# Performance work log

Measured on AMD Instinct MI355X. Metric: run time of the kernel, lower is better.

Reference implementation:

```python
import jax, jax.numpy as jnp
import numpy as np

STRIDE = 1
PAD = 1
DIL = 1


def setup_inputs() -> dict:
    key = jax.random.key(0)
    k1, k2, k3, k4 = jax.random.split(key, 4)
    N, Cin, H, W = 4, 256, 64, 64
    Cout, kh, kw = 256, 3, 3
    inputs = jax.random.normal(k1, (N, Cin, H, W), jnp.float32)
    filter = jax.random.normal(k2, (Cout, Cin, kh, kw), jnp.float32) * 0.05
    # offsets in pixels (y,x interleaved per tap), typical magnitude O(1)
    offset = jax.random.normal(k3, (N, 2 * kh * kw, H, W), jnp.float32)
    # modulation mask in [0,1) (post-sigmoid in real nets)
    mask = jax.random.uniform(k4, (N, kh * kw, H, W), jnp.float32)
    return {"inputs": inputs, "filter": filter, "offset": offset, "mask": mask}


def _dcn_forward(inputs, filt, offset, mask):
    N, C, H, W = inputs.shape
    Cout, _, kh, kw = filt.shape
    K = kh * kw
    Ho = (H + 2 * PAD - DIL * (kh - 1) - 1) // STRIDE + 1
    Wo = (W + 2 * PAD - DIL * (kw - 1) - 1) // STRIDE + 1

    # base sampling grid per kernel tap: [K, Ho, Wo]
    ki, kj = jnp.meshgrid(jnp.arange(kh), jnp.arange(kw), indexing='ij')
    ki = ki.reshape(K, 1, 1)
    kj = kj.reshape(K, 1, 1)
    base_y = (jnp.arange(Ho)[None, :, None] * STRIDE - PAD + ki * DIL).astype(jnp.float32)
    base_x = (jnp.arange(Wo)[None, None, :] * STRIDE - PAD + kj * DIL).astype(jnp.float32)

    # offset channels: per tap k, channel 2k = dy, channel 2k+1 = dx
    off = offset.reshape(N, K, 2, Ho, Wo)
    y = base_y[None] + off[:, :, 0]  # [N, K, Ho, Wo]
    x = base_x[None] + off[:, :, 1]

    y0 = jnp.floor(y)
    x0 = jnp.floor(x)
    ly = y - y0  # fractional parts, [N, K, Ho, Wo]
    lx = x - x0
    y0i = y0.astype(jnp.int32)
    x0i = x0.astype(jnp.int32)

    def gather(img, yy, xx):
        # img [C,H,W]; yy,xx [K,Ho,Wo] int; zero outside bounds
        valid = (yy >= 0) & (yy < H) & (xx >= 0) & (xx < W)
        yc = jnp.clip(yy, 0, H - 1)
        xc = jnp.clip(xx, 0, W - 1)
        return img[:, yc, xc] * valid.astype(img.dtype)  # [C,K,Ho,Wo]

    def sample_one(img, y0i, x0i, ly, lx):
        v00 = gather(img, y0i, x0i)
        v01 = gather(img, y0i, x0i + 1)
        v10 = gather(img, y0i + 1, x0i)
        v11 = gather(img, y0i + 1, x0i + 1)
        return (v00 * (1 - ly) * (1 - lx) + v01 * (1 - ly) * lx
                + v10 * ly * (1 - lx) + v11 * ly * lx)

    # bilinear-sampled, modulated im2col columns: [N, C, K, Ho, Wo]
    col = jax.vmap(sample_one)(inputs, y0i, x0i, ly, lx)
    col = col * mask.reshape(N, 1, K, Ho, Wo)

    # grouped conv with num_groups=1: plain GEMM over (C, K)
    out = jnp.einsum('ock,nckhw->nohw', filt.reshape(Cout, C, K), col)
    return out


def reference(inputs, filter, offset, mask):
    return _dcn_forward(inputs, filter, offset, mask)
```

## Files before the change

### kernel.cpp

```cpp
#include <hip/hip_runtime.h>
#include <stdint.h>

typedef __attribute__((ext_vector_type(2))) float f32x2;
typedef __attribute__((ext_vector_type(4))) float f32x4;
typedef __attribute__((ext_vector_type(8))) short bf16x8;

static constexpr int N_ = 4, C_ = 256, HW_ = 4096;
static constexpr int CO_ = 256, KTAP = 9, KK = 2304;
static constexpr int NSTEP = 72;
static constexpr int A_STEP_BYTES = 16 * 64 * 16;

static constexpr size_t NHWC_BYTES = (size_t)N_ * HW_ * C_ * 2;
static constexpr size_t ABF_OFF    = NHWC_BYTES;
static constexpr size_t ABF_BYTES  = (size_t)NSTEP * A_STEP_BYTES;

__device__ inline unsigned f2bf(float f) {
  unsigned u = __builtin_bit_cast(unsigned, f);
  unsigned r = u + 0x7FFFu + ((u >> 16) & 1u);
  return r >> 16;
}
__device__ inline float asf(unsigned u) { return __builtin_bit_cast(float, u); }

__global__ __launch_bounds__(256) void k_nchw_to_nhwc(const float* __restrict__ in,
                                                      unsigned short* __restrict__ nhwc) {
  __shared__ float tile[64][65];
  int b = blockIdx.x;
  int n = b >> 8, cg = (b >> 6) & 3, hwg = b & 63;
  int c0 = cg * 64, hw0 = hwg * 64;
  int t = threadIdx.x;
  int col = t & 63, r0 = t >> 6;
#pragma unroll
  for (int i = 0; i < 16; ++i) {
    int row = r0 + i * 4;
    tile[row][col] = in[(size_t)(n * C_ + c0 + row) * HW_ + hw0 + col];
  }
  __syncthreads();
  int pr = t >> 2, cc0 = (t & 3) * 16;
  unsigned us[8];
#pragma unroll
  for (int i = 0; i < 8; ++i) {
    unsigned lo = f2bf(tile[cc0 + 2 * i][pr]);
    unsigned hi = f2bf(tile[cc0 + 2 * i + 1][pr]);
    us[i] = lo | (hi << 16);
  }
  unsigned* dst = (unsigned*)(nhwc + (size_t)(n * HW_ + hw0 + pr) * C_ + c0 + cc0);
  ((uint4*)dst)[0] = make_uint4(us[0], us[1], us[2], us[3]);
  ((uint4*)dst)[1] = make_uint4(us[4], us[5], us[6], us[7]);
}

__global__ __launch_bounds__(256) void k_prep_filter(const float* __restrict__ filt,
                                                     unsigned short* __restrict__ abf2) {
  int gid = blockIdx.x * 256 + threadIdx.x;
  int o = gid >> 8, c = gid & 255;
  const float* f = filt + (size_t)(o * C_ + c) * KTAP;
  int rb = o >> 4;
  int lane = ((c >> 3) & 3) * 16 + (o & 15);
  int j = c & 7;
#pragma unroll
  for (int tap = 0; tap < KTAP; ++tap) {
    int s = tap * 8 + (c >> 5);
    abf2[((size_t)(s * 16 + rb) * 64 + lane) * 8 + j] = (unsigned short)f2bf(f[tap]);
  }
}

struct GB { uint4 g[4]; f32x4 w; };

__device__ __forceinline__ f32x2 unpk(unsigned u) {
  return (f32x2){asf(u << 16), asf(u & 0xffff0000u)};
}

__device__ __forceinline__ void buildB8(const GB& b, char* dst) {
  f32x2 r0 = b.w.x * unpk(b.g[0].x) + b.w.y * unpk(b.g[1].x) +
             b.w.z * unpk(b.g[2].x) + b.w.w * unpk(b.g[3].x);
  f32x2 r1 = b.w.x * unpk(b.g[0].y) + b.w.y * unpk(b.g[1].y) +
             b.w.z * unpk(b.g[2].y) + b.w.w * unpk(b.g[3].y);
  f32x2 r2 = b.w.x * unpk(b.g[0].z) + b.w.y * unpk(b.g[1].z) +
             b.w.z * unpk(b.g[2].z) + b.w.w * unpk(b.g[3].z);
  f32x2 r3 = b.w.x * unpk(b.g[0].w) + b.w.y * unpk(b.g[1].w) +
             b.w.z * unpk(b.g[2].w) + b.w.w * unpk(b.g[3].w);
  unsigned o0, o1, o2, o3;
  asm("v_cvt_pk_bf16_f32 %0, %1, %2" : "=v"(o0) : "v"(r0.x), "v"(r0.y));
  asm("v_cvt_pk_bf16_f32 %0, %1, %2" : "=v"(o1) : "v"(r1.x), "v"(r1.y));
  asm("v_cvt_pk_bf16_f32 %0, %1, %2" : "=v"(o2) : "v"(r2.x), "v"(r2.y));
  asm("v_cvt_pk_bf16_f32 %0, %1, %2" : "=v"(o3) : "v"(r3.x), "v"(r3.y));
  *(uint4*)dst = make_uint4(o0, o1, o2, o3);
}

#define MFMA_BF16 __builtin_amdgcn_mfma_f32_16x16x32_bf16

#define PIPE(S, RDP, WRP, GCON, GISS, AC0, AC1, AN0, AN1)                      \
  do {                                                                         \
    if (cons) {                                                                \
      int s1_ = (S) + 1 < NSTEP ? (S) + 1 : NSTEP - 1;                         \
      AN0 = *(const bf16x8*)(aoff0 + (size_t)s1_ * A_STEP_BYTES);              \
      AN1 = *(const bf16x8*)(aoff1 + (size_t)s1_ * A_STEP_BYTES);              \
      const char* bb_ = (const char*)&Bl[0][0] + (RDP) * 4096;                 \
      bf16x8 b0_ = *(const bf16x8*)(bb_ + bo0);                                \
      bf16x8 b1_ = *(const bf16x8*)(bb_ + bo1);                                \
      __builtin_amdgcn_s_setprio(1);                                           \
      acc[0][0] = MFMA_BF16(AC0, b0_, acc[0][0], 0, 0, 0);                     \
      acc[1][0] = MFMA_BF16(AC1, b0_, acc[1][0], 0, 0, 0);                     \
      acc[0][1] = MFMA_BF16(AC0, b1_, acc[0][1], 0, 0, 0);                     \
      acc[1][1] = MFMA_BF16(AC1, b1_, acc[1][1], 0, 0, 0);                     \
      __builtin_amdgcn_s_setprio(0);                                           \
      bf16x8 b2_ = *(const bf16x8*)(bb_ + bo2);                                \
      bf16x8 b3_ = *(const bf16x8*)(bb_ + bo3);                                \
      __builtin_amdgcn_s_setprio(1);                                           \
      acc[0][2] = MFMA_BF16(AC0, b2_, acc[0][2], 0, 0, 0);                     \
      acc[1][2] = MFMA_BF16(AC1, b2_, acc[1][2], 0, 0, 0);                     \
      acc[0][3] = MFMA_BF16(AC0, b3_, acc[0][3], 0, 0, 0);                     \
      acc[1][3] = MFMA_BF16(AC1, b3_, acc[1][3], 0, 0, 0);                     \
      __builtin_amdgcn_s_setprio(0);                                           \
    } else {                                                                   \
      int s2_ = (S) + 2 < NSTEP ? (S) + 2 : NSTEP - 1;                         \
      if ((s2_ & 7) == 0) {                                                    \
        int tp_ = s2_ >> 3;                                                    \
        uint4 ra_ = *(const uint4*)&recA[(tp_ * 64 + p_b) * 4];                \
        wS = *(const f32x4*)&recW[(tp_ * 64 + p_b) * 4];                       \
        vS.x = ra_.x + kq16; vS.y = ra_.y + kq16;                              \
        vS.z = ra_.z + kq16; vS.w = ra_.w + kq16;                              \
      }                                                                        \
      unsigned co_ = (unsigned)((s2_ & 7) * 64);                               \
      GISS.g[0] = *(const uint4*)(nb_u + vS.x + co_);                          \
      GISS.g[1] = *(const uint4*)(nb_u + vS.y + co_);                          \
      GISS.g[2] = *(const uint4*)(nb_u + vS.z + co_);                          \
      GISS.g[3] = *(const uint4*)(nb_u + vS.w + co_);                          \
      GISS.w = wS;                                                             \
      buildB8(GCON, bwp + (WRP) * 4096);                                       \
      asm volatile("s_waitcnt lgkmcnt(0)" ::: "memory");                       \
    }                                                                          \
    asm volatile("" ::: "memory");                                             \
    __builtin_amdgcn_s_barrier();                                              \
    asm volatile("" ::: "memory");                                             \
  } while (0)

__global__ __launch_bounds__(768, 3) void k_dcn_gemm(const unsigned short* __restrict__ nhwc,
                                                     const unsigned short* __restrict__ abf2,
                                                     const float* __restrict__ offs,
                                                     const float* __restrict__ msk,
                                                     float* __restrict__ out) {
  __shared__ __align__(16) unsigned short Bl[2][2048];
  __shared__ float recW[KTAP * 64 * 4];
  __shared__ unsigned recA[KTAP * 64 * 4];

  int bid = blockIdx.x;
  int b = ((bid & 7) << 5) | (bid >> 3);
  int n = b >> 6;
  int ho = b & 63;
  int hw0 = ho << 6;
  int t = threadIdx.x;

  for (int r = t; r < 576; r += 768) {
    int pl = r / 9;
    int tap = r - pl * 9;
    int hw = hw0 + pl;
    float dy = offs[(size_t)(n * 18 + 2 * tap) * HW_ + hw];
    float dx = offs[(size_t)(n * 18 + 2 * tap + 1) * HW_ + hw];
    float mk = msk[(size_t)(n * 9 + tap) * HW_ + hw];
    float y = (float)(ho - 1 + tap / 3) + dy;
    float x = (float)(pl - 1 + tap % 3) + dx;
    float fy = floorf(y), fx = floorf(x);
    float ly = y - fy, lx = x - fx;
    int y0 = (int)fy, x0 = (int)fx;
    int y1 = y0 + 1, x1 = x0 + 1;
    float vy0 = (y0 >= 0 && y0 < 64) ? 1.f : 0.f;
    float vy1 = (y1 >= 0 && y1 < 64) ? 1.f : 0.f;
    float vx0 = (x0 >= 0 && x0 < 64) ? 1.f : 0.f;
    float vx1 = (x1 >= 0 && x1 < 64) ? 1.f : 0.f;
    int y0c = min(max(y0, 0), 63), y1c = min(max(y1, 0), 63);
    int x0c = min(max(x0, 0), 63), x1c = min(max(x1, 0), 63);
    int base = (tap * 64 + pl) * 4;
    recW[base + 0] = (1.f - ly) * (1.f - lx) * mk * vy0 * vx0;
    recW[base + 1] = (1.f - ly) * lx * mk * vy0 * vx1;
    recW[base + 2] = ly * (1.f - lx) * mk * vy1 * vx0;
    recW[base + 3] = ly * lx * mk * vy1 * vx1;
    recA[base + 0] = (unsigned)((y0c * 64 + x0c) * 512);
    recA[base + 1] = (unsigned)((y0c * 64 + x1c) * 512);
    recA[base + 2] = (unsigned)((y1c * 64 + x0c) * 512);
    recA[base + 3] = (unsigned)((y1c * 64 + x1c) * 512);
  }
  __syncthreads();

  int lane = t & 63, wv = t >> 6;
  bool cons = wv < 8;

  const char* aoff0 = (const char*)abf2 + ((wv * 2 + 0) * 64 + lane) * 16;
  const char* aoff1 = aoff0 + 1024;
  int cqr = lane >> 4;
  int pxl = lane & 15;
  const int bo0 = cqr * 1024 + ((((0 * 16 + pxl) + cqr * 5) & 63) * 16);
  const int bo1 = cqr * 1024 + ((((1 * 16 + pxl) + cqr * 5) & 63) * 16);
  const int bo2 = cqr * 1024 + ((((2 * 16 + pxl) + cqr * 5) & 63) * 16);
  const int bo3 = cqr * 1024 + ((((3 * 16 + pxl) + cqr * 5) & 63) * 16);

  int p_b = (t >> 2) & 63;
  int kq = t & 3;
  unsigned kq16 = (unsigned)(kq * 16);
  const char* nb_u = (const char*)nhwc + (size_t)n * HW_ * C_ * 2;
  char* bwp = (char*)&Bl[0][0] + (kq * 1024 + ((p_b + kq * 5) & 63) * 16);

  f32x4 acc[2][4];
#pragma unroll
  for (int mi = 0; mi < 2; ++mi)
#pragma unroll
    for (int ni = 0; ni < 4; ++ni) acc[mi][ni] = (f32x4){0.f, 0.f, 0.f, 0.f};

  GB gA, gB;
  bf16x8 afc0, afc1, afn0, afn1;
  uint4 vS;
  f32x4 wS;

  if (cons) {
    afc0 = *(const bf16x8*)(aoff0);
    afc1 = *(const bf16x8*)(aoff1);
  } else {
    uint4 ra0 = *(const uint4*)&recA[p_b * 4];
    wS = *(const f32x4*)&recW[p_b * 4];
    vS.x = ra0.x + kq16; vS.y = ra0.y + kq16;
    vS.z = ra0.z + kq16; vS.w = ra0.w + kq16;
    gA.g[0] = *(const uint4*)(nb_u + vS.x);
    gA.g[1] = *(const uint4*)(nb_u + vS.y);
    gA.g[2] = *(const uint4*)(nb_u + vS.z);
    gA.g[3] = *(const uint4*)(nb_u + vS.w);
    gA.w = wS;
    gB.g[0] = *(const uint4*)(nb_u + vS.x + 64);
    gB.g[1] = *(const uint4*)(nb_u + vS.y + 64);
    gB.g[2] = *(const uint4*)(nb_u + vS.z + 64);
    gB.g[3] = *(const uint4*)(nb_u + vS.w + 64);
    gB.w = wS;
    buildB8(gA, bwp);
    asm volatile("s_waitcnt lgkmcnt(0)" ::: "memory");
  }
  asm volatile("" ::: "memory");
  __builtin_amdgcn_s_barrier();
  asm volatile("" ::: "memory");

  for (int s = 0; s < NSTEP; s += 2) {
    PIPE(s,     0, 1, gB, gA, afc0, afc1, afn0, afn1);
    PIPE(s + 1, 1, 0, gA, gB, afn0, afn1, afc0, afc1);
  }

  if (cons) {
    float* ob = out + (size_t)n * CO_ * HW_ + hw0;
#pragma unroll
    for (int mi = 0; mi < 2; ++mi)
#pragma unroll
      for (int ni = 0; ni < 4; ++ni)
#pragma unroll
        for (int jj = 0; jj < 4; ++jj) {
          int o = wv * 32 + mi * 16 + (lane >> 4) * 4 + jj;
          int hw = ni * 16 + (lane & 15);
          ob[(size_t)o * HW_ + hw] = acc[mi][ni][jj];
        }
  }
}

extern "C" void kernel_launch(void* const* d_in, const int* in_sizes, int n_in,
                              void* d_out, int out_size, void* d_ws, size_t ws_size,
                              hipStream_t stream) {
  const float* inp  = (const float*)d_in[0];
  const float* filt = (const float*)d_in[1];
  const float* offs = (const float*)d_in[2];
  const float* msk  = (const float*)d_in[3];
  float* out = (float*)d_out;
  if (ws_size < ABF_OFF + ABF_BYTES) return;
  unsigned short* nhwc = (unsigned short*)d_ws;
  unsigned short* abf2 = (unsigned short*)((char*)d_ws + ABF_OFF);

  k_nchw_to_nhwc<<<1024, 256, 0, stream>>>(inp, nhwc);
  k_prep_filter<<<256, 256, 0, stream>>>(filt, abf2);
  k_dcn_gemm<<<256, 768, 0, stream>>>(nhwc, abf2, offs, msk, out);
}
```

Measured before the change: 53.93 us.

## Split deformable sampling into separate kernel writing im2col to global memory

Adds a k_sample kernel that bilinearly samples and modulates the NHWC input into a global bf16 im2col buffer, then a k_gemm2 kernel that streams B tiles via global_load_lds into LDS and runs MFMA with 16 waves. The two prep kernels are merged into one launch, and the old fused kernel remains as a fallback when the workspace is too small. The aim is to decouple gather latency from the MFMA loop, at the cost of a large extra global write and read of the column buffer.

```diff
diff --git a/kernel.cpp b/kernel.cpp
--- a/kernel.cpp
+++ b/kernel.cpp
@@ -1,18 +1,24 @@
 #include <hip/hip_runtime.h>
 #include <stdint.h>
+
+#define AS1 __attribute__((address_space(1)))
+#define AS3 __attribute__((address_space(3)))
 
 typedef __attribute__((ext_vector_type(2))) float f32x2;
 typedef __attribute__((ext_vector_type(4))) float f32x4;
 typedef __attribute__((ext_vector_type(8))) short bf16x8;
 
 static constexpr int N_ = 4, C_ = 256, HW_ = 4096;
-static constexpr int CO_ = 256, KTAP = 9, KK = 2304;
+static constexpr int CO_ = 256, KTAP = 9;
 static constexpr int NSTEP = 72;
-static constexpr int A_STEP_BYTES = 16 * 64 * 16;
+static constexpr int A_PLANE = 16 * 64 * 16;
+static constexpr size_t TILE_STRIDE = 256 * 4096;
 
 static constexpr size_t NHWC_BYTES = (size_t)N_ * HW_ * C_ * 2;
 static constexpr size_t ABF_OFF    = NHWC_BYTES;
-static constexpr size_t ABF_BYTES  = (size_t)NSTEP * A_STEP_BYTES;
+static constexpr size_t ABF_BYTES  = (size_t)NSTEP * A_PLANE;
+static constexpr size_t BG_OFF     = ABF_OFF + ABF_BYTES;
+static constexpr size_t BG_BYTES   = (size_t)NSTEP * TILE_STRIDE;
 
 __device__ inline unsigned f2bf(float f) {
   unsigned u = __builtin_bit_cast(unsigned, f);
@@ -21,91 +27,225 @@
 }
 __device__ inline float asf(unsigned u) { return __builtin_bit_cast(float, u); }
 
-__global__ __launch_bounds__(256) void k_nchw_to_nhwc(const float* __restrict__ in,
-                                                      unsigned short* __restrict__ nhwc) {
-  __shared__ float tile[64][65];
+__global__ __launch_bounds__(256) void k_prep(const float* __restrict__ in,
+                                              const float* __restrict__ filt,
+                                              unsigned short* __restrict__ nhwc,
+                                              unsigned short* __restrict__ abf2) {
   int b = blockIdx.x;
-  int n = b >> 8, cg = (b >> 6) & 3, hwg = b & 63;
-  int c0 = cg * 64, hw0 = hwg * 64;
   int t = threadIdx.x;
-  int col = t & 63, r0 = t >> 6;
-#pragma unroll
-  for (int i = 0; i < 16; ++i) {
-    int row = r0 + i * 4;
-    tile[row][col] = in[(size_t)(n * C_ + c0 + row) * HW_ + hw0 + col];
-  }
-  __syncthreads();
-  int pr = t >> 2, cc0 = (t & 3) * 16;
-  unsigned us[8];
-#pragma unroll
-  for (int i = 0; i < 8; ++i) {
-    unsigned lo = f2bf(tile[cc0 + 2 * i][pr]);
-    unsigned hi = f2bf(tile[cc0 + 2 * i + 1][pr]);
-    us[i] = lo | (hi << 16);
-  }
-  unsigned* dst = (unsigned*)(nhwc + (size_t)(n * HW_ + hw0 + pr) * C_ + c0 + cc0);
-  ((uint4*)dst)[0] = make_uint4(us[0], us[1], us[2], us[3]);
-  ((uint4*)dst)[1] = make_uint4(us[4], us[5], us[6], us[7]);
-}
-
-__global__ __launch_bounds__(256) void k_prep_filter(const float* __restrict__ filt,
-                                                     unsigned short* __restrict__ abf2) {
-  int gid = blockIdx.x * 256 + threadIdx.x;
-  int o = gid >> 8, c = gid & 255;
-  const float* f = filt + (size_t)(o * C_ + c) * KTAP;
-  int rb = o >> 4;
-  int lane = ((c >> 3) & 3) * 16 + (o & 15);
-  int j = c & 7;
-#pragma unroll
-  for (int tap = 0; tap < KTAP; ++tap) {
-    int s = tap * 8 + (c >> 5);
-    abf2[((size_t)(s * 16 + rb) * 64 + lane) * 8 + j] = (unsigned short)f2bf(f[tap]);
-  }
-}
-
-struct GB { uint4 g[4]; f32x4 w; };
+  if (b < 1024) {
+    __shared__ float tile[64][65];
+    int n = b >> 8, cg = (b >> 6) & 3, hwg = b & 63;
+    int c0 = cg * 64, hw0 = hwg * 64;
+    int col = t & 63, r0 = t >> 6;
+#pragma unroll
+    for (int i = 0; i < 16; ++i) {
+      int row = r0 + i * 4;
+      tile[row][col] = in[(size_t)(n * C_ + c0 + row) * HW_ + hw0 + col];
+    }
+    __syncthreads();
+    int pr = t >> 2, cc0 = (t & 3) * 16;
+    unsigned us[8];
+#pragma unroll
+    for (int i = 0; i < 8; ++i) {
+      unsigned lo = f2bf(tile[cc0 + 2 * i][pr]);
+      unsigned hi = f2bf(tile[cc0 + 2 * i + 1][pr]);
+      us[i] = lo | (hi << 16);
+    }
+    unsigned* dst = (unsigned*)(nhwc + (size_t)(n * HW_ + hw0 + pr) * C_ + c0 + cc0);
+    ((uint4*)dst)[0] = make_uint4(us[0], us[1], us[2], us[3]);
+    ((uint4*)dst)[1] = make_uint4(us[4], us[5], us[6], us[7]);
+  } else {
+    int gid = (b - 1024) * 256 + t;
+    int o = gid >> 8, c = gid & 255;
+    const float* f = filt + (size_t)(o * C_ + c) * KTAP;
+    int rb = o >> 4;
+    int lane = ((c >> 3) & 3) * 16 + (o & 15);
+    int j = c & 7;
+#pragma unroll
+    for (int tap = 0; tap < KTAP; ++tap) {
+      int s = tap * 8 + (c >> 5);
+      abf2[((size_t)(s * 16 + rb) * 64 + lane) * 8 + j] = (unsigned short)f2bf(f[tap]);
+    }
+  }
+}
 
 __device__ __forceinline__ f32x2 unpk(unsigned u) {
   return (f32x2){asf(u << 16), asf(u & 0xffff0000u)};
 }
 
-__device__ __forceinline__ void buildB8(const GB& b, char* dst) {
-  f32x2 r0 = b.w.x * unpk(b.g[0].x) + b.w.y * unpk(b.g[1].x) +
-             b.w.z * unpk(b.g[2].x) + b.w.w * unpk(b.g[3].x);
-  f32x2 r1 = b.w.x * unpk(b.g[0].y) + b.w.y * unpk(b.g[1].y) +
-             b.w.z * unpk(b.g[2].y) + b.w.w * unpk(b.g[3].y);
-  f32x2 r2 = b.w.x * unpk(b.g[0].z) + b.w.y * unpk(b.g[1].z) +
-             b.w.z * unpk(b.g[2].z) + b.w.w * unpk(b.g[3].z);
-  f32x2 r3 = b.w.x * unpk(b.g[0].w) + b.w.y * unpk(b.g[1].w) +
-             b.w.z * unpk(b.g[2].w) + b.w.w * unpk(b.g[3].w);
+__device__ __forceinline__ uint4 comb8(const uint4& g0, const uint4& g1,
+                                       const uint4& g2, const uint4& g3, f32x4 w) {
+  f32x2 r0 = w.x * unpk(g0.x) + w.y * unpk(g1.x) + w.z * unpk(g2.x) + w.w * unpk(g3.x);
+  f32x2 r1 = w.x * unpk(g0.y) + w.y * unpk(g1.y) + w.z * unpk(g2.y) + w.w * unpk(g3.y);
+  f32x2 r2 = w.x * unpk(g0.z) + w.y * unpk(g1.z) + w.z * unpk(g2.z) + w.w * unpk(g3.z);
+  f32x2 r3 = w.x * unpk(g0.w) + w.y * unpk(g1.w) + w.z * unpk(g2.w) + w.w * unpk(g3.w);
   unsigned o0, o1, o2, o3;
   asm("v_cvt_pk_bf16_f32 %0, %1, %2" : "=v"(o0) : "v"(r0.x), "v"(r0.y));
   asm("v_cvt_pk_bf16_f32 %0, %1, %2" : "=v"(o1) : "v"(r1.x), "v"(r1.y));
   asm("v_cvt_pk_bf16_f32 %0, %1, %2" : "=v"(o2) : "v"(r2.x), "v"(r2.y));
   asm("v_cvt_pk_bf16_f32 %0, %1, %2" : "=v"(o3) : "v"(r3.x), "v"(r3.y));
-  *(uint4*)dst = make_uint4(o0, o1, o2, o3);
+  return make_uint4(o0, o1, o2, o3);
+}
+
+__global__ __launch_bounds__(512, 2) void k_sample(const unsigned short* __restrict__ nhwc,
+                                                   const float* __restrict__ offs,
+                                                   const float* __restrict__ msk,
+                                                   unsigned short* __restrict__ bglob) {
+  __shared__ f32x4 sW[64];
+  __shared__ uint4 sA[64];
+  int bid = blockIdx.x;
+  int b = (bid & 7) * 288 + (bid >> 3);
+  int row = b / 9, tap = b - row * 9;
+  int n = row >> 6, ho = row & 63;
+  int t = threadIdx.x;
+
+  if (t < 64) {
+    int pl = t, hw = ho * 64 + pl;
+    float dy = offs[(size_t)(n * 18 + 2 * tap) * HW_ + hw];
+    float dx = offs[(size_t)(n * 18 + 2 * tap + 1) * HW_ + hw];
+    float mk = msk[(size_t)(n * 9 + tap) * HW_ + hw];
+    float y = (float)(ho - 1 + tap / 3) + dy;
+    float x = (float)(pl - 1 + tap % 3) + dx;
+    float fy = floorf(y), fx = floorf(x);
+    float ly = y - fy, lx = x - fx;
+    int y0 = (int)fy, x0 = (int)fx;
+    int y1 = y0 + 1, x1 = x0 + 1;
+    float vy0 = (y0 >= 0 && y0 < 64) ? 1.f : 0.f;
+    float vy1 = (y1 >= 0 && y1 < 64) ? 1.f : 0.f;
+    float vx0 = (x0 >= 0 && x0 < 64) ? 1.f : 0.f;
+    float vx1 = (x1 >= 0 && x1 < 64) ? 1.f : 0.f;
+    int y0c = min(max(y0, 0), 63), y1c = min(max(y1, 0), 63);
+    int x0c = min(max(x0, 0), 63), x1c = min(max(x1, 0), 63);
+    sW[pl] = (f32x4){(1.f - ly) * (1.f - lx) * mk * vy0 * vx0,
+                     (1.f - ly) * lx * mk * vy0 * vx1,
+                     ly * (1.f - lx) * mk * vy1 * vx0,
+                     ly * lx * mk * vy1 * vx1};
+    sA[pl] = make_uint4((unsigned)((y0c * 64 + x0c) * 512),
+                        (unsigned)((y0c * 64 + x1c) * 512),
+                        (unsigned)((y1c * 64 + x0c) * 512),
+                        (unsigned)((y1c * 64 + x1c) * 512));
+  }
+  __syncthreads();
+
+  int px = t >> 3, cq = t & 7;
+  f32x4 w = sW[px];
+  uint4 ra = sA[px];
+  const char* nb = (const char*)nhwc + (size_t)n * HW_ * C_ * 2;
+  unsigned c16 = (unsigned)(cq * 16);
+
+  uint4 g0[4], g1[4], g2[4], g3[4];
+#pragma unroll
+  for (int j = 0; j < 4; ++j) {
+    unsigned o_ = (unsigned)(j * 128) + c16;
+    g0[j] = *(const uint4*)(nb + ra.x + o_);
+    g1[j] = *(const uint4*)(nb + ra.y + o_);
+    g2[j] = *(const uint4*)(nb + ra.z + o_);
+    g3[j] = *(const uint4*)(nb + ra.w + o_);
+  }
+
+  char* outb = (char*)bglob + (size_t)row * 4096 + px * 64 + (cq & 3) * 16;
+  int sbase = tap * 8 + (cq >> 2);
+#pragma unroll
+  for (int j = 0; j < 4; ++j) {
+    uint4 o4 = comb8(g0[j], g1[j], g2[j], g3[j], w);
+    *(uint4*)(outb + (size_t)(sbase + j * 2) * TILE_STRIDE) = o4;
+  }
 }
 
 #define MFMA_BF16 __builtin_amdgcn_mfma_f32_16x16x32_bf16
 
-#define PIPE(S, RDP, WRP, GCON, GISS, AC0, AC1, AN0, AN1)                      \
+#define GSTEP(S, P)                                                            \
+  do {                                                                         \
+    int s1_ = (S) + 1 < NSTEP ? (S) + 1 : NSTEP - 1;                           \
+    if (wv < 4) {                                                              \
+      const char* src_ = bg + (size_t)s1_ * TILE_STRIDE + wv * 1024 + lane * 16; \
+      __builtin_amdgcn_global_load_lds((const AS1 void*)src_,                  \
+          (AS3 void*)((char*)&Bl[0][0] + ((P) ^ 1) * 4096 + wv * 1024 + lane * 16), \
+          16, 0, 0);                                                           \
+    }                                                                          \
+    afn = *(const bf16x8*)(aoff + (size_t)s1_ * A_PLANE);                      \
+    {                                                                          \
+      const char* bb_ = (const char*)&Bl[0][0] + (P) * 4096;                   \
+      bf16x8 b0_ = *(const bf16x8*)(bb_ + bo0);                                \
+      bf16x8 b1_ = *(const bf16x8*)(bb_ + bo1);                                \
+      bf16x8 b2_ = *(const bf16x8*)(bb_ + bo2);                                \
+      bf16x8 b3_ = *(const bf16x8*)(bb_ + bo3);                                \
+      __builtin_amdgcn_s_setprio(1);                                           \
+      acc[0] = MFMA_BF16(afc, b0_, acc[0], 0, 0, 0);                           \
+      acc[1] = MFMA_BF16(afc, b1_, acc[1], 0, 0, 0);                           \
+      acc[2] = MFMA_BF16(afc, b2_, acc[2], 0, 0, 0);                           \
+      acc[3] = MFMA_BF16(afc, b3_, acc[3], 0, 0, 0);                           \
+      __builtin_amdgcn_s_setprio(0);                                           \
+    }                                                                          \
+    __syncthreads();                                                           \
+    afc = afn;                                                                 \
+  } while (0)
+
+__global__ __launch_bounds__(1024, 4) void k_gemm2(const unsigned short* __restrict__ bglob,
+                                                   const unsigned short* __restrict__ abf2,
+                                                   float* __restrict__ out) {
+  __shared__ __align__(16) unsigned short Bl[2][2048];
+  int bid = blockIdx.x;
+  int b = ((bid & 7) << 5) | (bid >> 3);
+  int n = b >> 6, ho = b & 63, hw0 = ho << 6;
+  int t = threadIdx.x, lane = t & 63, wv = t >> 6;
+
+  const char* aoff = (const char*)abf2 + ((size_t)(wv * 64 + lane)) * 16;
+  const char* bg = (const char*)bglob + (size_t)b * 4096;
+  int pxl = lane & 15, kq = lane >> 4;
+  const int bo0 = 0 * 1024 + pxl * 64 + kq * 16;
+  const int bo1 = 1 * 1024 + pxl * 64 + kq * 16;
+  const int bo2 = 2 * 1024 + pxl * 64 + kq * 16;
+  const int bo3 = 3 * 1024 + pxl * 64 + kq * 16;
+
+  f32x4 acc[4];
+#pragma unroll
+  for (int ni = 0; ni < 4; ++ni) acc[ni] = (f32x4){0.f, 0.f, 0.f, 0.f};
+
+  bf16x8 afc, afn;
+  if (wv < 4) {
+    const char* src = bg + wv * 1024 + lane * 16;
+    __builtin_amdgcn_global_load_lds((const AS1 void*)src,
+        (AS3 void*)((char*)&Bl[0][0] + wv * 1024 + lane * 16), 16, 0, 0);
+  }
+  afc = *(const bf16x8*)(aoff);
+  __syncthreads();
+
+  for (int s = 0; s < NSTEP; s += 2) {
+    GSTEP(s, 0);
+    GSTEP(s + 1, 1);
+  }
+
+  float* ob = out + (size_t)n * CO_ * HW_ + hw0;
+#pragma unroll
+  for (int ni = 0; ni < 4; ++ni)
+#pragma unroll
+    for (int jj = 0; jj < 4; ++jj) {
+      int o = wv * 16 + kq * 4 + jj;
+      int hw = ni * 16 + pxl;
+      ob[(size_t)o * HW_ + hw] = acc[ni][jj];
+    }
+}
+
+struct GB { uint4 g[4]; f32x4 w; };
+
+#define FPIPE(S, RDP, WRP, GCON, GISS, AC0, AC1, AN0, AN1)                     \
   do {                                                                         \
     if (cons) {                                                                \
       int s1_ = (S) + 1 < NSTEP ? (S) + 1 : NSTEP - 1;                         \
-      AN0 = *(const bf16x8*)(aoff0 + (size_t)s1_ * A_STEP_BYTES);              \
-      AN1 = *(const bf16x8*)(aoff1 + (size_t)s1_ * A_STEP_BYTES);              \
+      AN0 = *(const bf16x8*)(faoff0 + (size_t)s1_ * A_PLANE);                  \
+      AN1 = *(const bf16x8*)(faoff0 + 1024 + (size_t)s1_ * A_PLANE);           \
       const char* bb_ = (const char*)&Bl[0][0] + (RDP) * 4096;                 \
-      bf16x8 b0_ = *(const bf16x8*)(bb_ + bo0);                                \
-      bf16x8 b1_ = *(const bf16x8*)(bb_ + bo1);                                \
+      bf16x8 b0_ = *(const bf16x8*)(bb_ + fbo0);                               \
+      bf16x8 b1_ = *(const bf16x8*)(bb_ + fbo1);                               \
+      bf16x8 b2_ = *(const bf16x8*)(bb_ + fbo2);                               \
+      bf16x8 b3_ = *(const bf16x8*)(bb_ + fbo3);                               \
       __builtin_amdgcn_s_setprio(1);                                           \
       acc[0][0] = MFMA_BF16(AC0, b0_, acc[0][0], 0, 0, 0);                     \
       acc[1][0] = MFMA_BF16(AC1, b0_, acc[1][0], 0, 0, 0);                     \
       acc[0][1] = MFMA_BF16(AC0, b1_, acc[0][1], 0, 0, 0);                     \
       acc[1][1] = MFMA_BF16(AC1, b1_, acc[1][1], 0, 0, 0);                     \
-      __builtin_amdgcn_s_setprio(0);                                           \
-      bf16x8 b2_ = *(const bf16x8*)(bb_ + bo2);                                \
-      bf16x8 b3_ = *(const bf16x8*)(bb_ + bo3);                                \
-      __builtin_amdgcn_s_setprio(1);                                           \
       acc[0][2] = MFMA_BF16(AC0, b2_, acc[0][2], 0, 0, 0);                     \
       acc[1][2] = MFMA_BF16(AC1, b2_, acc[1][2], 0, 0, 0);                     \
       acc[0][3] = MFMA_BF16(AC0, b3_, acc[0][3], 0, 0, 0);                     \
@@ -126,7 +266,8 @@
       GISS.g[2] = *(const uint4*)(nb_u + vS.z + co_);                          \
       GISS.g[3] = *(const uint4*)(nb_u + vS.w + co_);                          \
       GISS.w = wS;                                                             \
-      buildB8(GCON, bwp + (WRP) * 4096);                                       \
+      uint4 o4_ = comb8(GCON.g[0], GCON.g[1], GCON.g[2], GCON.g[3], GCON.w);   \
+      *(uint4*)(bwp + (WRP) * 4096) = o4_;                                     \
       asm volatile("s_waitcnt lgkmcnt(0)" ::: "memory");                       \
     }                                                                          \
     asm volatile("" ::: "memory");                                             \
@@ -134,20 +275,18 @@
     asm volatile("" ::: "memory");                                             \
   } while (0)
 
-__global__ __launch_bounds__(768, 3) void k_dcn_gemm(const unsigned short* __restrict__ nhwc,
-                                                     const unsigned short* __restrict__ abf2,
-                                                     const float* __restrict__ offs,
-                                                     const float* __restrict__ msk,
-                                                     float* __restrict__ out) {
+__global__ __launch_bounds__(768, 3) void k_fused(const unsigned short* __restrict__ nhwc,
+                                                  const unsigned short* __restrict__ abf2,
+                                                  const float* __restrict__ offs,
+                                                  const float* __restrict__ msk,
+                                                  float* __restrict__ out) {
   __shared__ __align__(16) unsigned short Bl[2][2048];
   __shared__ float recW[KTAP * 64 * 4];
   __shared__ unsigned recA[KTAP * 64 * 4];
 
   int bid = blockIdx.x;
   int b = ((bid & 7) << 5) | (bid >> 3);
-  int n = b >> 6;
-  int ho = b & 63;
-  int hw0 = ho << 6;
+  int n = b >> 6, ho = b & 63, hw0 = ho << 6;
   int t = threadIdx.x;
 
   for (int r = t; r < 576; r += 768) {
@@ -184,20 +323,19 @@
   int lane = t & 63, wv = t >> 6;
   bool cons = wv < 8;
 
-  const char* aoff0 = (const char*)abf2 + ((wv * 2 + 0) * 64 + lane) * 16;
-  const char* aoff1 = aoff0 + 1024;
-  int cqr = lane >> 4;
-  int pxl = lane & 15;
-  const int bo0 = cqr * 1024 + ((((0 * 16 + pxl) + cqr * 5) & 63) * 16);
-  const int bo1 = cqr * 1024 + ((((1 * 16 + pxl) + cqr * 5) & 63) * 16);
-  const int bo2 = cqr * 1024 + ((((2 * 16 + pxl) + cqr * 5) & 63) * 16);
-  const int bo3 = cqr * 1024 + ((((3 * 16 + pxl) + cqr * 5) & 63) * 16);
-
-  int p_b = (t >> 2) & 63;
-  int kq = t & 3;
+  const char* faoff0 = (const char*)abf2 + ((wv * 2) * 64 + lane) * 16;
+  int p_r = lane >> 4, pxl = lane & 15;
+  const int fbo0 = p_r * 1024 + (((pxl + 0) + 5 * p_r) & 63) * 16;
+  const int fbo1 = p_r * 1024 + (((pxl + 16) + 5 * p_r) & 63) * 16;
+  const int fbo2 = p_r * 1024 + (((pxl + 32) + 5 * p_r) & 63) * 16;
+  const int fbo3 = p_r * 1024 + (((pxl + 48) + 5 * p_r) & 63) * 16;
+
+  int pid = t - 512;
+  int p_b = (pid >> 2) & 63;
+  int kq = pid & 3;
   unsigned kq16 = (unsigned)(kq * 16);
   const char* nb_u = (const char*)nhwc + (size_t)n * HW_ * C_ * 2;
-  char* bwp = (char*)&Bl[0][0] + (kq * 1024 + ((p_b + kq * 5) & 63) * 16);
+  char* bwp = (char*)&Bl[0][0] + kq * 1024 + ((p_b + 5 * kq) & 63) * 16;
 
   f32x4 acc[2][4];
 #pragma unroll
@@ -211,8 +349,8 @@
   f32x4 wS;
 
   if (cons) {
-    afc0 = *(const bf16x8*)(aoff0);
-    afc1 = *(const bf16x8*)(aoff1);
+    afc0 = *(const bf16x8*)(faoff0);
+    afc1 = *(const bf16x8*)(faoff0 + 1024);
   } else {
     uint4 ra0 = *(const uint4*)&recA[p_b * 4];
     wS = *(const f32x4*)&recW[p_b * 4];
@@ -228,7 +366,8 @@
     gB.g[2] = *(const uint4*)(nb_u + vS.z + 64);
     gB.g[3] = *(const uint4*)(nb_u + vS.w + 64);
     gB.w = wS;
-    buildB8(gA, bwp);
+    uint4 o4 = comb8(gA.g[0], gA.g[1], gA.g[2], gA.g[3], gA.w);
+    *(uint4*)(bwp) = o4;
     asm volatile("s_waitcnt lgkmcnt(0)" ::: "memory");
   }
   asm volatile("" ::: "memory");
@@ -236,8 +375,8 @@
   asm volatile("" ::: "memory");
 
   for (int s = 0; s < NSTEP; s += 2) {
-    PIPE(s,     0, 1, gB, gA, afc0, afc1, afn0, afn1);
-    PIPE(s + 1, 1, 0, gA, gB, afn0, afn1, afc0, afc1);
+    FPIPE(s,     0, 1, gB, gA, afc0, afc1, afn0, afn1);
+    FPIPE(s + 1, 1, 0, gA, gB, afn0, afn1, afc0, afc1);
   }
 
   if (cons) {
@@ -267,7 +406,12 @@
   unsigned short* nhwc = (unsigned short*)d_ws;
   unsigned short* abf2 = (unsigned short*)((char*)d_ws + ABF_OFF);
 
-  k_nchw_to_nhwc<<<1024, 256, 0, stream>>>(inp, nhwc);
-  k_prep_filter<<<256, 256, 0, stream>>>(filt, abf2);
-  k_dcn_gemm<<<256, 768, 0, stream>>>(nhwc, abf2, offs, msk, out);
-}
+  k_prep<<<1280, 256, 0, stream>>>(inp, filt, nhwc, abf2);
+  if (ws_size >= BG_OFF + BG_BYTES) {
+    unsigned short* bglob = (unsigned short*)((char*)d_ws + BG_OFF);
+    k_sample<<<2304, 512, 0, stream>>>(nhwc, offs, msk, bglob);
+    k_gemm2<<<256, 1024, 0, stream>>>(bglob, abf2, out);
+  } else {
+    k_fused<<<256, 768, 0, stream>>>(nhwc, abf2, offs, msk, out);
+  }
+}
```

New measurement: 68.08 us. +26.2%, slower.
